# Optimization experiments

Hardware: AMD Instinct MI355X
Metric: run time of the kernel (lower is better)

## Reference

```python
import jax, jax.numpy as jnp
import numpy as np

DT = 0.01


def _mlp(x, W1, b1, W2, b2, W3, b3):
    # Linear -> tanh -> Linear -> tanh -> Linear
    h = jnp.tanh(x @ W1 + b1)
    h = jnp.tanh(h @ W2 + b2)
    return h @ W3 + b3


def setup_inputs() -> dict:
    B, T, D, H, F = 512, 128, 512, 1024, 128
    key = jax.random.key(0)
    ks = jax.random.split(key, 20)

    def lin(kw, kb, fan_in, fan_out):
        W = jax.random.normal(kw, (fan_in, fan_out), jnp.float32) / jnp.sqrt(jnp.float32(fan_in))
        b = jnp.zeros((fan_out,), jnp.float32)
        return W, b

    window = jax.random.normal(ks[0], (B, T, D), jnp.float32)
    eW1, eb1 = lin(ks[1], ks[2], D, H)
    eW2, eb2 = lin(ks[3], ks[4], H, H)
    eW3, eb3 = lin(ks[5], ks[6], H, F)
    dW1, db1 = lin(ks[7], ks[8], F, H)
    dW2, db2 = lin(ks[9], ks[10], H, H)
    dW3, db3 = lin(ks[11], ks[12], H, D)
    kW1, kb1 = lin(ks[13], ks[14], F, F)  # koopman_dim -> 2*num_eigenvalues == F
    kW2, kb2 = lin(ks[15], ks[16], F, F)
    return {
        'window': window,
        'eW1': eW1, 'eb1': eb1, 'eW2': eW2, 'eb2': eb2, 'eW3': eW3, 'eb3': eb3,
        'dW1': dW1, 'db1': db1, 'dW2': dW2, 'db2': db2, 'dW3': dW3, 'db3': db3,
        'kW1': kW1, 'kb1': kb1, 'kW2': kW2, 'kb2': kb2,
    }


def _koopman(z0, T, kW1, kb1, kW2, kb2):
    # parameterization: Linear -> tanh -> Linear, producing (mu, omega) per eigen-pair
    B, F = z0.shape
    n_eig = F // 2
    p = jnp.tanh(z0 @ kW1 + kb1) @ kW2 + kb2          # [B, 2*n_eig]
    p = p.reshape(B, n_eig, 2)
    mu, omega = p[..., 0], p[..., 1]
    exp_mu = jnp.exp(mu * DT)
    c = jnp.cos(omega * DT)
    s = jnp.sin(omega * DT)
    # per-sample 2x2 rotation-scaling blocks: [B, n_eig, 2, 2]
    blocks = jnp.stack([
        jnp.stack([exp_mu * c, -exp_mu * s], axis=-1),
        jnp.stack([exp_mu * s, exp_mu * c], axis=-1),
    ], axis=-2)

    def step(z, _):
        zp = z.reshape(B, n_eig, 2)
        zn = jnp.einsum('bnij,bnj->bni', blocks, zp).reshape(B, F)
        return zn, zn

    _, preds = jax.lax.scan(step, z0, None, length=T)  # [T, B, F]
    return jnp.transpose(preds, (1, 0, 2))             # [B, T, F]


def reference(window, eW1, eb1, eW2, eb2, eW3, eb3,
              dW1, db1, dW2, db2, dW3, db3,
              kW1, kb1, kW2, kb2):
    x0 = window[:, 0, :]          # [B, D]
    targets = window[:, 1:, :]    # [B, T-1, D]
    T = targets.shape[1]

    z0 = _mlp(x0, eW1, eb1, eW2, eb2, eW3, eb3)          # [B, F]
    x0_recon = _mlp(z0, dW1, db1, dW2, db2, dW3, db3)    # [B, D]
    z_pred = _koopman(z0, T, kW1, kb1, kW2, kb2)         # [B, T-1, F]
    x_pred = _mlp(z_pred, dW1, db1, dW2, db2, dW3, db3)  # [B, T-1, D]
    z_true = _mlp(targets, eW1, eb1, eW2, eb2, eW3, eb3) # [B, T-1, F]

    loss_recon = jnp.mean((x0_recon - x0) ** 2)
    loss_linear = jnp.mean((z_pred - z_true) ** 2)
    loss_pred = jnp.mean((x_pred - targets) ** 2)
    total = loss_recon + loss_linear + loss_pred
    return total, loss_recon, loss_linear, loss_pred
```

## Files before the change

### kernel.cpp

```cpp
#include <hip/hip_runtime.h>
#include <cstddef>
#include <cstdint>


#define KDT 0.01f
#define CH 16384
#define NCHUNK 4

typedef _Float16 f16;
typedef f16 f16x8 __attribute__((ext_vector_type(8)));
typedef f16 f16x4 __attribute__((ext_vector_type(4)));
typedef float f32x4 __attribute__((ext_vector_type(4)));

typedef __attribute__((address_space(1))) const unsigned int gu32;
typedef __attribute__((address_space(3))) unsigned int lu32;

__device__ __forceinline__ void gl_lds16(const void* g, void* l) {
    __builtin_amdgcn_global_load_lds((gu32*)g, (lu32*)l, 16, 0, 0);
}

__device__ __forceinline__ float fast_tanh(float x) {
    x = fminf(fmaxf(x, -15.f), 15.f);
    const float e = __expf(2.f * x);
    return (e - 1.f) / (e + 1.f);
}

#define PB_LIN 0
#define PB_REC 4096
#define PB_PRED 6144
#define PB_TOTAL 8192

template <int MODE, bool TANH, bool OUTF16>
__global__ __launch_bounds__(256) void k_gemm_f16(const f16* __restrict__ A,
                                                  const f16* __restrict__ Wt,
                                                  const float* __restrict__ bias,
                                                  void* __restrict__ Cv,
                                                  int M, int N, int K,
                                                  const float* __restrict__ win,
                                                  int g0,
                                                  double* __restrict__ p0,
                                                  double* __restrict__ p1)
{
    __shared__ __align__(16) f16 As[128][32];
    __shared__ __align__(16) f16 Bs[128][32];
    __shared__ double sm[256];

    const int t  = threadIdx.x;
    const int l  = t & 63;
    const int wv = t >> 6;
    const int wr = wv >> 1, wc = wv & 1;
    const int lm = l & 15, lk = l >> 4;
    const int bm = blockIdx.y, bn = blockIdx.x;

    const f16* Ab = A  + (size_t)bm * 128 * K;
    const f16* Bb = Wt + (size_t)bn * 128 * K;
    char* sA = (char*)&As[0][0];
    char* sB = (char*)&Bs[0][0];
    const int wbase = wv * 64;

    f32x4 acc[4][4] = {};

    for (int k0 = 0; k0 < K; k0 += 32) {
#pragma unroll
        for (int r = 0; r < 2; ++r) {
            const int c = r * 256 + t;
            const size_t goff = (size_t)(c >> 2) * K + (size_t)k0 + (size_t)(c & 3) * 8;
            gl_lds16(Ab + goff, sA + (size_t)(r * 256 + wbase) * 16);
            gl_lds16(Bb + goff, sB + (size_t)(r * 256 + wbase) * 16);
        }
        __syncthreads();

        f16x8 af[4], bf[4];
#pragma unroll
        for (int i = 0; i < 4; ++i) {
            af[i] = *reinterpret_cast<const f16x8*>(&As[wr * 64 + i * 16 + lm][lk * 8]);
            bf[i] = *reinterpret_cast<const f16x8*>(&Bs[wc * 64 + i * 16 + lm][lk * 8]);
        }
#pragma unroll
        for (int i = 0; i < 4; ++i)
#pragma unroll
            for (int j = 0; j < 4; ++j)
                acc[i][j] = __builtin_amdgcn_mfma_f32_16x16x32_f16(af[i], bf[j], acc[i][j], 0, 0, 0);
        __syncthreads();
    }

    const int col0 = bn * 128 + wc * 64;

    if (MODE == 0) {
        const int row0 = bm * 128 + wr * 64;
#pragma unroll
        for (int j = 0; j < 4; ++j) {
            const int col = col0 + j * 16 + lm;
            const float bv = bias[col];
#pragma unroll
            for (int i = 0; i < 4; ++i)
#pragma unroll
                for (int q = 0; q < 4; ++q) {
                    const int row = row0 + i * 16 + lk * 4 + q;
                    float v = acc[i][j][q] + bv;
                    if (TANH) v = fast_tanh(v);
                    if (OUTF16) ((f16*)Cv)[(size_t)row * N + col] = (f16)v;
                    else        ((float*)Cv)[(size_t)row * N + col] = v;
                }
        }
    } else {
        double s0 = 0.0, s1 = 0.0;
#pragma unroll
        for (int i = 0; i < 4; ++i) {
#pragma unroll
            for (int q = 0; q < 4; ++q) {
                const int rl = bm * 128 + wr * 64 + i * 16 + lk * 4 + q;
                const int g  = g0 + rl;
                const int tt = g & 127;
#pragma unroll
                for (int j = 0; j < 4; ++j) {
                    const int col = col0 + j * 16 + lm;
                    const float v = acc[i][j][q] + bias[col];
                    const float d = v - win[(size_t)g * 512 + col];
                    if (tt == 0) s0 += (double)d * d;
                    else         s1 += (double)d * d;
                }
            }
        }
        const int bid = blockIdx.y * gridDim.x + blockIdx.x;
        sm[t] = s0;
        __syncthreads();
        for (int o = 128; o > 0; o >>= 1) {
            if (t < o) sm[t] += sm[t + o];
            __syncthreads();
        }
        if (t == 0) p0[bid] = sm[0];
        __syncthreads();
        sm[t] = s1;
        __syncthreads();
        for (int o = 128; o > 0; o >>= 1) {
            if (t < o) sm[t] += sm[t + o];
            __syncthreads();
        }
        if (t == 0) p1[bid] = sm[0];
    }
}

__global__ __launch_bounds__(256) void k_wt(const float* __restrict__ W,
                                            f16* __restrict__ Wt, int K, int N)
{
    __shared__ float tl[32][33];
    const int n0 = blockIdx.x * 32, k0 = blockIdx.y * 32;
    const int tx = threadIdx.x & 31, ty = threadIdx.x >> 5;
#pragma unroll
    for (int i = 0; i < 32; i += 8)
        tl[ty + i][tx] = W[(size_t)(k0 + ty + i) * N + n0 + tx];
    __syncthreads();
#pragma unroll
    for (int i = 0; i < 32; i += 8)
        Wt[(size_t)(n0 + ty + i) * K + k0 + tx] = (f16)tl[tx][ty + i];
}

__global__ __launch_bounds__(256) void k_gather_all(const float* __restrict__ win,
                                                    f16* __restrict__ out, int g0)
{
    const int i = blockIdx.x * 256 + threadIdx.x;
    if (i >= CH * 64) return;
    const int r = i >> 6, c8 = i & 63;
    const float* s = win + ((size_t)(g0 + r)) * 512 + c8 * 8;
    const float4 v0 = *reinterpret_cast<const float4*>(s);
    const float4 v1 = *reinterpret_cast<const float4*>(s + 4);
    f16x8 o;
    o[0] = (f16)v0.x; o[1] = (f16)v0.y; o[2] = (f16)v0.z; o[3] = (f16)v0.w;
    o[4] = (f16)v1.x; o[5] = (f16)v1.y; o[6] = (f16)v1.z; o[7] = (f16)v1.w;
    *reinterpret_cast<f16x8*>(out + (size_t)r * 512 + c8 * 8) = o;
}

__global__ __launch_bounds__(256) void k_gather_z0(const float* __restrict__ cZfull,
                                                   float* __restrict__ z0f32,
                                                   f16* __restrict__ z0f16)
{
    const int i = blockIdx.x * 256 + threadIdx.x;
    if (i >= 512 * 32) return;
    const int b = i >> 5, c4 = i & 31;
    const float4 v = *reinterpret_cast<const float4*>(cZfull + (size_t)b * 16384 + c4 * 4);
    *reinterpret_cast<float4*>(z0f32 + (size_t)b * 128 + c4 * 4) = v;
    f16x4 o;
    o[0] = (f16)v.x; o[1] = (f16)v.y; o[2] = (f16)v.z; o[3] = (f16)v.w;
    *reinterpret_cast<f16x4*>(z0f16 + (size_t)b * 128 + c4 * 4) = o;
}

__global__ __launch_bounds__(256) void k_koop(const float* __restrict__ cZ,
                                              const float* __restrict__ z0,
                                              const float* __restrict__ pK,
                                              int g0,
                                              f16* __restrict__ decin,
                                              double* __restrict__ p0)
{
    const int idx = blockIdx.x * 256 + threadIdx.x;
    const int r = idx >> 4, c8 = idx & 15;
    const int g = g0 + r;
    const int tt = g & 127;
    const int bb = g >> 7;

    float zt[8];
    *reinterpret_cast<float4*>(zt)     = *reinterpret_cast<const float4*>(cZ + (size_t)r * 128 + c8 * 8);
    *reinterpret_cast<float4*>(zt + 4) = *reinterpret_cast<const float4*>(cZ + (size_t)r * 128 + c8 * 8 + 4);

    double s = 0.0;
    float ov[8];
    if (tt == 0) {
#pragma unroll
        for (int k = 0; k < 8; ++k) ov[k] = zt[k];
    } else {
        float zz[8], qq[8];
        *reinterpret_cast<float4*>(zz)     = *reinterpret_cast<const float4*>(z0 + (size_t)bb * 128 + c8 * 8);
        *reinterpret_cast<float4*>(zz + 4) = *reinterpret_cast<const float4*>(z0 + (size_t)bb * 128 + c8 * 8 + 4);
        *reinterpret_cast<float4*>(qq)     = *reinterpret_cast<const float4*>(pK + (size_t)bb * 128 + c8 * 8);
        *reinterpret_cast<float4*>(qq + 4) = *reinterpret_cast<const float4*>(pK + (size_t)bb * 128 + c8 * 8 + 4);
        const float tf = KDT * (float)tt;
#pragma unroll
        for (int pr = 0; pr < 4; ++pr) {
            const float e = __expf(qq[2 * pr] * tf);
            float sn, cs;
            __sincosf(qq[2 * pr + 1] * tf, &sn, &cs);
            const float zx = zz[2 * pr], zy = zz[2 * pr + 1];
            const float a = e * (cs * zx - sn * zy);
            const float b = e * (sn * zx + cs * zy);
            ov[2 * pr] = a; ov[2 * pr + 1] = b;
            const float d0 = a - zt[2 * pr], d1 = b - zt[2 * pr + 1];
            s += (double)d0 * d0 + (double)d1 * d1;
        }
    }
    f16x8 o;
#pragma unroll
    for (int k = 0; k < 8; ++k) o[k] = (f16)ov[k];
    *reinterpret_cast<f16x8*>(decin + (size_t)r * 128 + c8 * 8) = o;

    __shared__ double sm[256];
    sm[threadIdx.x] = s;
    __syncthreads();
    for (int off = 128; off > 0; off >>= 1) {
        if (threadIdx.x < (unsigned)off) sm[threadIdx.x] += sm[threadIdx.x + off];
        __syncthreads();
    }
    if (threadIdx.x == 0) p0[blockIdx.x] = sm[0];
}

__global__ __launch_bounds__(256) void k_finalize(const double* __restrict__ pb,
                                                  float* __restrict__ out)
{
    __shared__ double sm[256];
    const int t = threadIdx.x;
    double a0 = 0.0, a1 = 0.0, a2 = 0.0;
    for (int i = t; i < 4096; i += 256) a0 += pb[PB_LIN + i];
    for (int i = t; i < 2048; i += 256) a1 += pb[PB_REC + i];
    for (int i = t; i < 2048; i += 256) a2 += pb[PB_PRED + i];

    double r[3];
    double v[3] = {a0, a1, a2};
    for (int k = 0; k < 3; ++k) {
        sm[t] = v[k];
        __syncthreads();
        for (int o = 128; o > 0; o >>= 1) {
            if (t < o) sm[t] += sm[t + o];
            __syncthreads();
        }
        r[k] = sm[0];
        __syncthreads();
    }
    if (t == 0) {
        const double linear = r[0] / (65024.0 * 128.0);
        const double recon  = r[1] / (512.0 * 512.0);
        const double pred   = r[2] / (65024.0 * 512.0);
        out[0] = (float)(recon + linear + pred);
        out[1] = (float)recon;
        out[2] = (float)linear;
        out[3] = (float)pred;
    }
}

extern "C" void kernel_launch(void* const* d_in, const int* in_sizes, int n_in,
                              void* d_out, int out_size, void* d_ws, size_t ws_size,
                              hipStream_t stream)
{
    const float* window = (const float*)d_in[0];
    const float* eW1 = (const float*)d_in[1];
    const float* eb1 = (const float*)d_in[2];
    const float* eW2 = (const float*)d_in[3];
    const float* eb2 = (const float*)d_in[4];
    const float* eW3 = (const float*)d_in[5];
    const float* eb3 = (const float*)d_in[6];
    const float* dW1 = (const float*)d_in[7];
    const float* db1 = (const float*)d_in[8];
    const float* dW2 = (const float*)d_in[9];
    const float* db2 = (const float*)d_in[10];
    const float* dW3 = (const float*)d_in[11];
    const float* db3 = (const float*)d_in[12];
    const float* kW1 = (const float*)d_in[13];
    const float* kb1 = (const float*)d_in[14];
    const float* kW2 = (const float*)d_in[15];
    const float* kb2 = (const float*)d_in[16];
    float* out = (float*)d_out;
    (void)in_sizes; (void)n_in; (void)out_size; (void)ws_size;

    char* p = (char*)d_ws;
    size_t off = 0;
    auto takeB = [&](size_t bytes) -> char* {
        char* r = p + off;
        off += (bytes + 255) & ~(size_t)255;
        return r;
    };
    double* pb = (double*)takeB(PB_TOTAL * 8);
    f16* eW1t = (f16*)takeB((size_t)512 * 1024 * 2);
    f16* eW2t = (f16*)takeB((size_t)1024 * 1024 * 2);
    f16* eW3t = (f16*)takeB((size_t)1024 * 128 * 2);
    f16* dW1t = (f16*)takeB((size_t)128 * 1024 * 2);
    f16* dW2t = (f16*)takeB((size_t)1024 * 1024 * 2);
    f16* dW3t = (f16*)takeB((size_t)1024 * 512 * 2);
    f16* kW1t = (f16*)takeB((size_t)128 * 128 * 2);
    f16* kW2t = (f16*)takeB((size_t)128 * 128 * 2);
    float* z0f32 = (float*)takeB((size_t)65536 * 4);
    f16* z0f16 = (f16*)takeB((size_t)65536 * 2);
    f16* hK = (f16*)takeB((size_t)65536 * 2);
    float* pKbuf = (float*)takeB((size_t)65536 * 4);
    float* cZfull = (float*)takeB((size_t)65536 * 128 * 4);
    f16* cIn = (f16*)takeB((size_t)CH * 512 * 2);
    f16* cH1 = (f16*)takeB((size_t)CH * 1024 * 2);
    f16* cH2 = (f16*)takeB((size_t)CH * 1024 * 2);
    f16* decin = (f16*)takeB((size_t)CH * 128 * 2);

    hipMemsetAsync(pb, 0, PB_TOTAL * 8, stream);

    auto G = [&](const f16* A, const f16* Wt, const float* b, void* C,
                 int M, int N, int K, bool tanh_, bool f16out) {
        dim3 grid(N / 128, M / 128);
        if (tanh_)       k_gemm_f16<0, true,  true ><<<grid, 256, 0, stream>>>(A, Wt, b, C, M, N, K, nullptr, 0, nullptr, nullptr);
        else if (f16out) k_gemm_f16<0, false, true ><<<grid, 256, 0, stream>>>(A, Wt, b, C, M, N, K, nullptr, 0, nullptr, nullptr);
        else             k_gemm_f16<0, false, false><<<grid, 256, 0, stream>>>(A, Wt, b, C, M, N, K, nullptr, 0, nullptr, nullptr);
    };
    auto WT = [&](const float* W, f16* Wt, int K, int N) {
        k_wt<<<dim3(N / 32, K / 32), 256, 0, stream>>>(W, Wt, K, N);
    };

    WT(eW1, eW1t, 512, 1024);  WT(eW2, eW2t, 1024, 1024); WT(eW3, eW3t, 1024, 128);
    WT(dW1, dW1t, 128, 1024);  WT(dW2, dW2t, 1024, 1024); WT(dW3, dW3t, 1024, 512);
    WT(kW1, kW1t, 128, 128);   WT(kW2, kW2t, 128, 128);

    for (int c = 0; c < NCHUNK; ++c) {
        const int g0 = c * CH;
        k_gather_all<<<CH * 64 / 256, 256, 0, stream>>>(window, cIn, g0);
        G(cIn, eW1t, eb1, cH1, CH, 1024, 512, true, true);
        G(cH1, eW2t, eb2, cH2, CH, 1024, 1024, true, true);
        G(cH2, eW3t, eb3, cZfull + (size_t)g0 * 128, CH, 128, 1024, false, false);
    }

    k_gather_z0<<<64, 256, 0, stream>>>(cZfull, z0f32, z0f16);
    G(z0f16, kW1t, kb1, hK, 512, 128, 128, true, true);
    G(hK,    kW2t, kb2, pKbuf, 512, 128, 128, false, false);

    for (int c = 0; c < NCHUNK; ++c) {
        const int g0 = c * CH;
        k_koop<<<CH * 16 / 256, 256, 0, stream>>>(cZfull + (size_t)g0 * 128, z0f32, pKbuf,
                                                  g0, decin, pb + PB_LIN + c * 1024);
        G(decin, dW1t, db1, cH1, CH, 1024, 128, true, true);
        G(cH1,   dW2t, db2, cH2, CH, 1024, 1024, true, true);
        k_gemm_f16<2, false, false><<<dim3(4, CH / 128), 256, 0, stream>>>(
            cH2, dW3t, db3, nullptr, CH, 512, 1024,
            window, g0, pb + PB_REC + c * 512, pb + PB_PRED + c * 512);
    }

    k_finalize<<<1, 256, 0, stream>>>(pb, out);
}
```

Baseline: 1.284 ms.

## Add 256x256 double-buffered swizzled MFMA GEMM and single-chunk execution

Introduces a new 256x256-tile GEMM kernel with 512 threads, XOR-swizzled LDS layout, double-buffered global-to-LDS prefetch interleaved with MFMA phases, s_setprio around the MFMA blocks, and grid remapping for cache locality. It is used for the large encoder and decoder layers, including the fused loss epilogue. When the workspace is large enough, the whole batch runs as one chunk instead of four. The aim is more data reuse per tile, overlap of loads with compute, and fewer launches, at the cost of higher register and LDS pressure and lower occupancy.

```diff
diff --git a/kernel.cpp b/kernel.cpp
--- a/kernel.cpp
+++ b/kernel.cpp
@@ -4,8 +4,6 @@
 
 
 #define KDT 0.01f
-#define CH 16384
-#define NCHUNK 4
 
 typedef _Float16 f16;
 typedef f16 f16x8 __attribute__((ext_vector_type(8)));
@@ -30,20 +28,187 @@
 #define PB_PRED 6144
 #define PB_TOTAL 8192
 
+
+__device__ __forceinline__ void stage256(const f16* __restrict__ g, char* ldsDst,
+                                         int t, int K, int kk)
+{
+#pragma unroll
+    for (int r = 0; r < 4; ++r) {
+        const int row = r * 64 + (t >> 3);
+        const int sc = ((t & 7) ^ (row & 7)) * 8;
+        gl_lds16(g + (size_t)row * K + kk + sc, ldsDst + row * 128 + (t & 7) * 16);
+    }
+}
+
+template <int MH, int NH>
+__device__ __forceinline__ void phase_mfma(f32x4 (&acc)[8][4], const char* sA, const char* sB,
+                                           int wm, int wn, int lm, int lk)
+{
+    f16x8 af[4][2], bf[2][2];
+#pragma unroll
+    for (int i = 0; i < 4; ++i)
+#pragma unroll
+        for (int ks = 0; ks < 2; ++ks) {
+            const int row = wm * 128 + (MH * 4 + i) * 16 + lm;
+            const int slot = (ks * 4 + lk) ^ (lm & 7);
+            af[i][ks] = *(const f16x8*)(sA + row * 128 + slot * 16);
+        }
+#pragma unroll
+    for (int j = 0; j < 2; ++j)
+#pragma unroll
+        for (int ks = 0; ks < 2; ++ks) {
+            const int row = wn * 64 + (NH * 2 + j) * 16 + lm;
+            const int slot = (ks * 4 + lk) ^ (lm & 7);
+            bf[j][ks] = *(const f16x8*)(sB + row * 128 + slot * 16);
+        }
+    __builtin_amdgcn_s_setprio(1);
+#pragma unroll
+    for (int i = 0; i < 4; ++i)
+#pragma unroll
+        for (int j = 0; j < 2; ++j)
+#pragma unroll
+            for (int ks = 0; ks < 2; ++ks)
+                acc[MH * 4 + i][NH * 2 + j] = __builtin_amdgcn_mfma_f32_16x16x32_f16(
+                    af[i][ks], bf[j][ks], acc[MH * 4 + i][NH * 2 + j], 0, 0, 0);
+    __builtin_amdgcn_s_setprio(0);
+}
+
+template <bool PREF>
+__device__ __forceinline__ void run_tile(f32x4 (&acc)[8][4], char* sbase, int buf,
+                                         const f16* __restrict__ Ab, const f16* __restrict__ Bb,
+                                         int t, int K, int kkNext, int wm, int wn, int lm, int lk)
+{
+    const char* sA = sbase + buf * 32768;
+    const char* sB = sbase + 65536 + buf * 32768;
+    char* dA = sbase + (buf ^ 1) * 32768;
+    char* dB = sbase + 65536 + (buf ^ 1) * 32768;
+    phase_mfma<0, 0>(acc, sA, sB, wm, wn, lm, lk);
+    if (PREF) stage256(Ab, dA, t, K, kkNext);
+    phase_mfma<0, 1>(acc, sA, sB, wm, wn, lm, lk);
+    if (PREF) stage256(Bb, dB, t, K, kkNext);
+    phase_mfma<1, 0>(acc, sA, sB, wm, wn, lm, lk);
+    phase_mfma<1, 1>(acc, sA, sB, wm, wn, lm, lk);
+}
+
 template <int MODE, bool TANH, bool OUTF16>
+__global__ __launch_bounds__(512, 2) void k_gemm256(const f16* __restrict__ A,
+                                                    const f16* __restrict__ Wt,
+                                                    const float* __restrict__ bias,
+                                                    void* __restrict__ Cv,
+                                                    int M, int N, int K,
+                                                    const float* __restrict__ win,
+                                                    int g0,
+                                                    double* __restrict__ p0,
+                                                    double* __restrict__ p1)
+{
+    __shared__ __align__(16) f16 lds[65536];
+    char* sbase = (char*)lds;
+
+    const int t  = threadIdx.x;
+    const int l  = t & 63;
+    const int wid = t >> 6;
+    const int wm = wid >> 2, wn = wid & 3;
+    const int lm = l & 15, lk = l >> 4;
+
+    const int gx = gridDim.x;
+    const int nwg = gx * gridDim.y;
+    const int orig = blockIdx.y * gx + blockIdx.x;
+    const int cpx = nwg >> 3;
+    const int tile = (orig & 7) * cpx + (orig >> 3);
+    const int bm = tile / gx;
+    const int bn = tile % gx;
+
+    const f16* Ab = A  + (size_t)bm * 256 * K;
+    const f16* Bb = Wt + (size_t)bn * 256 * K;
+    const int nt = K >> 6;
+
+    f32x4 acc[8][4] = {};
+
+    stage256(Ab, sbase, t, K, 0);
+    stage256(Bb, sbase + 65536, t, K, 0);
+    __syncthreads();
+
+    for (int kt = 0; kt < nt; kt += 2) {
+        run_tile<true>(acc, sbase, 0, Ab, Bb, t, K, (kt + 1) << 6, wm, wn, lm, lk);
+        __syncthreads();
+        if (kt + 2 < nt) {
+            run_tile<true>(acc, sbase, 1, Ab, Bb, t, K, (kt + 2) << 6, wm, wn, lm, lk);
+            __syncthreads();
+        } else {
+            run_tile<false>(acc, sbase, 1, Ab, Bb, t, K, 0, wm, wn, lm, lk);
+        }
+    }
+
+    const int row0g = bm * 256 + wm * 128;
+    const int col0g = bn * 256 + wn * 64;
+
+    if (MODE == 0) {
+#pragma unroll
+        for (int n = 0; n < 4; ++n) {
+            const int col = col0g + n * 16 + lm;
+            const float bv = bias[col];
+#pragma unroll
+            for (int m = 0; m < 8; ++m)
+#pragma unroll
+                for (int q = 0; q < 4; ++q) {
+                    const int row = row0g + m * 16 + lk * 4 + q;
+                    float v = acc[m][n][q] + bv;
+                    if (TANH) v = fast_tanh(v);
+                    if (OUTF16) ((f16*)Cv)[(size_t)row * N + col] = (f16)v;
+                    else        ((float*)Cv)[(size_t)row * N + col] = v;
+                }
+        }
+    } else {
+        double s0 = 0.0, s1 = 0.0;
+        float bv[4];
+#pragma unroll
+        for (int n = 0; n < 4; ++n) bv[n] = bias[col0g + n * 16 + lm];
+#pragma unroll
+        for (int m = 0; m < 8; ++m)
+#pragma unroll
+            for (int q = 0; q < 4; ++q) {
+                const int rl = row0g + m * 16 + lk * 4 + q;
+                const int g  = g0 + rl;
+                const int tt = g & 127;
+#pragma unroll
+                for (int n = 0; n < 4; ++n) {
+                    const int col = col0g + n * 16 + lm;
+                    const float v = acc[m][n][q] + bv[n];
+                    const float d = v - win[(size_t)g * 512 + col];
+                    if (tt == 0) s0 += (double)d * d;
+                    else         s1 += (double)d * d;
+                }
+            }
+        __syncthreads();
+        double* dsm = (double*)lds;
+        const int slot = (g0 / 256 + bm) * gx + bn;
+        dsm[t] = s0;
+        __syncthreads();
+        for (int o = 256; o > 0; o >>= 1) {
+            if (t < o) dsm[t] += dsm[t + o];
+            __syncthreads();
+        }
+        if (t == 0) p0[slot] = dsm[0];
+        __syncthreads();
+        dsm[t] = s1;
+        __syncthreads();
+        for (int o = 256; o > 0; o >>= 1) {
+            if (t < o) dsm[t] += dsm[t + o];
+            __syncthreads();
+        }
+        if (t == 0) p1[slot] = dsm[0];
+    }
+}
+
+template <bool TANH, bool OUTF16>
 __global__ __launch_bounds__(256) void k_gemm_f16(const f16* __restrict__ A,
                                                   const f16* __restrict__ Wt,
                                                   const float* __restrict__ bias,
                                                   void* __restrict__ Cv,
-                                                  int M, int N, int K,
-                                                  const float* __restrict__ win,
-                                                  int g0,
-                                                  double* __restrict__ p0,
-                                                  double* __restrict__ p1)
+                                                  int M, int N, int K)
 {
     __shared__ __align__(16) f16 As[128][32];
     __shared__ __align__(16) f16 Bs[128][32];
-    __shared__ double sm[256];
 
     const int t  = threadIdx.x;
     const int l  = t & 63;
@@ -84,60 +249,22 @@
         __syncthreads();
     }
 
+    const int row0 = bm * 128 + wr * 64;
     const int col0 = bn * 128 + wc * 64;
-
-    if (MODE == 0) {
-        const int row0 = bm * 128 + wr * 64;
-#pragma unroll
-        for (int j = 0; j < 4; ++j) {
-            const int col = col0 + j * 16 + lm;
-            const float bv = bias[col];
-#pragma unroll
-            for (int i = 0; i < 4; ++i)
-#pragma unroll
-                for (int q = 0; q < 4; ++q) {
-                    const int row = row0 + i * 16 + lk * 4 + q;
-                    float v = acc[i][j][q] + bv;
-                    if (TANH) v = fast_tanh(v);
-                    if (OUTF16) ((f16*)Cv)[(size_t)row * N + col] = (f16)v;
-                    else        ((float*)Cv)[(size_t)row * N + col] = v;
-                }
-        }
-    } else {
-        double s0 = 0.0, s1 = 0.0;
-#pragma unroll
-        for (int i = 0; i < 4; ++i) {
+#pragma unroll
+    for (int j = 0; j < 4; ++j) {
+        const int col = col0 + j * 16 + lm;
+        const float bv = bias[col];
+#pragma unroll
+        for (int i = 0; i < 4; ++i)
 #pragma unroll
             for (int q = 0; q < 4; ++q) {
-                const int rl = bm * 128 + wr * 64 + i * 16 + lk * 4 + q;
-                const int g  = g0 + rl;
-                const int tt = g & 127;
-#pragma unroll
-                for (int j = 0; j < 4; ++j) {
-                    const int col = col0 + j * 16 + lm;
-                    const float v = acc[i][j][q] + bias[col];
-                    const float d = v - win[(size_t)g * 512 + col];
-                    if (tt == 0) s0 += (double)d * d;
-                    else         s1 += (double)d * d;
-                }
+                const int row = row0 + i * 16 + lk * 4 + q;
+                float v = acc[i][j][q] + bv;
+                if (TANH) v = fast_tanh(v);
+                if (OUTF16) ((f16*)Cv)[(size_t)row * N + col] = (f16)v;
+                else        ((float*)Cv)[(size_t)row * N + col] = v;
             }
-        }
-        const int bid = blockIdx.y * gridDim.x + blockIdx.x;
-        sm[t] = s0;
-        __syncthreads();
-        for (int o = 128; o > 0; o >>= 1) {
-            if (t < o) sm[t] += sm[t + o];
-            __syncthreads();
-        }
-        if (t == 0) p0[bid] = sm[0];
-        __syncthreads();
-        sm[t] = s1;
-        __syncthreads();
-        for (int o = 128; o > 0; o >>= 1) {
-            if (t < o) sm[t] += sm[t + o];
-            __syncthreads();
-        }
-        if (t == 0) p1[bid] = sm[0];
     }
 }
 
@@ -157,10 +284,10 @@
 }
 
 __global__ __launch_bounds__(256) void k_gather_all(const float* __restrict__ win,
-                                                    f16* __restrict__ out, int g0)
+                                                    f16* __restrict__ out, int g0, int nrows)
 {
     const int i = blockIdx.x * 256 + threadIdx.x;
-    if (i >= CH * 64) return;
+    if (i >= nrows * 64) return;
     const int r = i >> 6, c8 = i & 63;
     const float* s = win + ((size_t)(g0 + r)) * 512 + c8 * 8;
     const float4 v0 = *reinterpret_cast<const float4*>(s);
@@ -188,49 +315,51 @@
 __global__ __launch_bounds__(256) void k_koop(const float* __restrict__ cZ,
                                               const float* __restrict__ z0,
                                               const float* __restrict__ pK,
-                                              int g0,
+                                              int g0, int nrows,
                                               f16* __restrict__ decin,
                                               double* __restrict__ p0)
 {
     const int idx = blockIdx.x * 256 + threadIdx.x;
-    const int r = idx >> 4, c8 = idx & 15;
-    const int g = g0 + r;
-    const int tt = g & 127;
-    const int bb = g >> 7;
-
-    float zt[8];
-    *reinterpret_cast<float4*>(zt)     = *reinterpret_cast<const float4*>(cZ + (size_t)r * 128 + c8 * 8);
-    *reinterpret_cast<float4*>(zt + 4) = *reinterpret_cast<const float4*>(cZ + (size_t)r * 128 + c8 * 8 + 4);
-
     double s = 0.0;
-    float ov[8];
-    if (tt == 0) {
-#pragma unroll
-        for (int k = 0; k < 8; ++k) ov[k] = zt[k];
-    } else {
-        float zz[8], qq[8];
-        *reinterpret_cast<float4*>(zz)     = *reinterpret_cast<const float4*>(z0 + (size_t)bb * 128 + c8 * 8);
-        *reinterpret_cast<float4*>(zz + 4) = *reinterpret_cast<const float4*>(z0 + (size_t)bb * 128 + c8 * 8 + 4);
-        *reinterpret_cast<float4*>(qq)     = *reinterpret_cast<const float4*>(pK + (size_t)bb * 128 + c8 * 8);
-        *reinterpret_cast<float4*>(qq + 4) = *reinterpret_cast<const float4*>(pK + (size_t)bb * 128 + c8 * 8 + 4);
-        const float tf = KDT * (float)tt;
-#pragma unroll
-        for (int pr = 0; pr < 4; ++pr) {
-            const float e = __expf(qq[2 * pr] * tf);
-            float sn, cs;
-            __sincosf(qq[2 * pr + 1] * tf, &sn, &cs);
-            const float zx = zz[2 * pr], zy = zz[2 * pr + 1];
-            const float a = e * (cs * zx - sn * zy);
-            const float b = e * (sn * zx + cs * zy);
-            ov[2 * pr] = a; ov[2 * pr + 1] = b;
-            const float d0 = a - zt[2 * pr], d1 = b - zt[2 * pr + 1];
-            s += (double)d0 * d0 + (double)d1 * d1;
-        }
-    }
-    f16x8 o;
-#pragma unroll
-    for (int k = 0; k < 8; ++k) o[k] = (f16)ov[k];
-    *reinterpret_cast<f16x8*>(decin + (size_t)r * 128 + c8 * 8) = o;
+    if (idx < nrows * 16) {
+        const int r = idx >> 4, c8 = idx & 15;
+        const int g = g0 + r;
+        const int tt = g & 127;
+        const int bb = g >> 7;
+
+        float zt[8];
+        *reinterpret_cast<float4*>(zt)     = *reinterpret_cast<const float4*>(cZ + (size_t)r * 128 + c8 * 8);
+        *reinterpret_cast<float4*>(zt + 4) = *reinterpret_cast<const float4*>(cZ + (size_t)r * 128 + c8 * 8 + 4);
+
+        float ov[8];
+        if (tt == 0) {
+#pragma unroll
+            for (int k = 0; k < 8; ++k) ov[k] = zt[k];
+        } else {
+            float zz[8], qq[8];
+            *reinterpret_cast<float4*>(zz)     = *reinterpret_cast<const float4*>(z0 + (size_t)bb * 128 + c8 * 8);
+            *reinterpret_cast<float4*>(zz + 4) = *reinterpret_cast<const float4*>(z0 + (size_t)bb * 128 + c8 * 8 + 4);
+            *reinterpret_cast<float4*>(qq)     = *reinterpret_cast<const float4*>(pK + (size_t)bb * 128 + c8 * 8);
+            *reinterpret_cast<float4*>(qq + 4) = *reinterpret_cast<const float4*>(pK + (size_t)bb * 128 + c8 * 8 + 4);
+            const float tf = KDT * (float)tt;
+#pragma unroll
+            for (int pr = 0; pr < 4; ++pr) {
+                const float e = __expf(qq[2 * pr] * tf);
+                float sn, cs;
+                __sincosf(qq[2 * pr + 1] * tf, &sn, &cs);
+                const float zx = zz[2 * pr], zy = zz[2 * pr + 1];
+                const float a = e * (cs * zx - sn * zy);
+                const float b = e * (sn * zx + cs * zy);
+                ov[2 * pr] = a; ov[2 * pr + 1] = b;
+                const float d0 = a - zt[2 * pr], d1 = b - zt[2 * pr + 1];
+                s += (double)d0 * d0 + (double)d1 * d1;
+            }
+        }
+        f16x8 o;
+#pragma unroll
+        for (int k = 0; k < 8; ++k) o[k] = (f16)ov[k];
+        *reinterpret_cast<f16x8*>(decin + (size_t)r * 128 + c8 * 8) = o;
+    }
 
     __shared__ double sm[256];
     sm[threadIdx.x] = s;
@@ -297,7 +426,10 @@
     const float* kW2 = (const float*)d_in[15];
     const float* kb2 = (const float*)d_in[16];
     float* out = (float*)d_out;
-    (void)in_sizes; (void)n_in; (void)out_size; (void)ws_size;
+    (void)in_sizes; (void)n_in; (void)out_size;
+
+    const int nch = (ws_size >= (450ull << 20)) ? 1 : 4;
+    const int MC  = 65536 / nch;
 
     char* p = (char*)d_ws;
     size_t off = 0;
@@ -320,19 +452,26 @@
     f16* hK = (f16*)takeB((size_t)65536 * 2);
     float* pKbuf = (float*)takeB((size_t)65536 * 4);
     float* cZfull = (float*)takeB((size_t)65536 * 128 * 4);
-    f16* cIn = (f16*)takeB((size_t)CH * 512 * 2);
-    f16* cH1 = (f16*)takeB((size_t)CH * 1024 * 2);
-    f16* cH2 = (f16*)takeB((size_t)CH * 1024 * 2);
-    f16* decin = (f16*)takeB((size_t)CH * 128 * 2);
+    f16* aIn  = (f16*)takeB((size_t)MC * 512 * 2);
+    f16* cH1  = (f16*)takeB((size_t)MC * 1024 * 2);
+    f16* cH2  = (f16*)takeB((size_t)MC * 1024 * 2);
+    f16* decin = (f16*)takeB((size_t)MC * 128 * 2);
 
     hipMemsetAsync(pb, 0, PB_TOTAL * 8, stream);
 
-    auto G = [&](const f16* A, const f16* Wt, const float* b, void* C,
-                 int M, int N, int K, bool tanh_, bool f16out) {
+    auto G256 = [&](const f16* A, const f16* Wt, const float* b, void* C,
+                    int M, int N, int K, bool tanh_, bool f16out) {
+        dim3 grid(N / 256, M / 256);
+        if (tanh_)       k_gemm256<0, true,  true ><<<grid, 512, 0, stream>>>(A, Wt, b, C, M, N, K, nullptr, 0, nullptr, nullptr);
+        else if (f16out) k_gemm256<0, false, true ><<<grid, 512, 0, stream>>>(A, Wt, b, C, M, N, K, nullptr, 0, nullptr, nullptr);
+        else             k_gemm256<0, false, false><<<grid, 512, 0, stream>>>(A, Wt, b, C, M, N, K, nullptr, 0, nullptr, nullptr);
+    };
+    auto G128 = [&](const f16* A, const f16* Wt, const float* b, void* C,
+                    int M, int N, int K, bool tanh_, bool f16out) {
         dim3 grid(N / 128, M / 128);
-        if (tanh_)       k_gemm_f16<0, true,  true ><<<grid, 256, 0, stream>>>(A, Wt, b, C, M, N, K, nullptr, 0, nullptr, nullptr);
-        else if (f16out) k_gemm_f16<0, false, true ><<<grid, 256, 0, stream>>>(A, Wt, b, C, M, N, K, nullptr, 0, nullptr, nullptr);
-        else             k_gemm_f16<0, false, false><<<grid, 256, 0, stream>>>(A, Wt, b, C, M, N, K, nullptr, 0, nullptr, nullptr);
+        if (tanh_)       k_gemm_f16<true,  true ><<<grid, 256, 0, stream>>>(A, Wt, b, C, M, N, K);
+        else if (f16out) k_gemm_f16<false, true ><<<grid, 256, 0, stream>>>(A, Wt, b, C, M, N, K);
+        else             k_gemm_f16<false, false><<<grid, 256, 0, stream>>>(A, Wt, b, C, M, N, K);
     };
     auto WT = [&](const float* W, f16* Wt, int K, int N) {
         k_wt<<<dim3(N / 32, K / 32), 256, 0, stream>>>(W, Wt, K, N);
@@ -342,27 +481,27 @@
     WT(dW1, dW1t, 128, 1024);  WT(dW2, dW2t, 1024, 1024); WT(dW3, dW3t, 1024, 512);
     WT(kW1, kW1t, 128, 128);   WT(kW2, kW2t, 128, 128);
 
-    for (int c = 0; c < NCHUNK; ++c) {
-        const int g0 = c * CH;
-        k_gather_all<<<CH * 64 / 256, 256, 0, stream>>>(window, cIn, g0);
-        G(cIn, eW1t, eb1, cH1, CH, 1024, 512, true, true);
-        G(cH1, eW2t, eb2, cH2, CH, 1024, 1024, true, true);
-        G(cH2, eW3t, eb3, cZfull + (size_t)g0 * 128, CH, 128, 1024, false, false);
+    for (int c = 0; c < nch; ++c) {
+        const int g0 = c * MC;
+        k_gather_all<<<MC * 64 / 256, 256, 0, stream>>>(window, aIn, g0, MC);
+        G256(aIn, eW1t, eb1, cH1, MC, 1024, 512, true, true);
+        G256(cH1, eW2t, eb2, cH2, MC, 1024, 1024, true, true);
+        G128(cH2, eW3t, eb3, cZfull + (size_t)g0 * 128, MC, 128, 1024, false, false);
     }
 
     k_gather_z0<<<64, 256, 0, stream>>>(cZfull, z0f32, z0f16);
-    G(z0f16, kW1t, kb1, hK, 512, 128, 128, true, true);
-    G(hK,    kW2t, kb2, pKbuf, 512, 128, 128, false, false);
-
-    for (int c = 0; c < NCHUNK; ++c) {
-        const int g0 = c * CH;
-        k_koop<<<CH * 16 / 256, 256, 0, stream>>>(cZfull + (size_t)g0 * 128, z0f32, pKbuf,
-                                                  g0, decin, pb + PB_LIN + c * 1024);
-        G(decin, dW1t, db1, cH1, CH, 1024, 128, true, true);
-        G(cH1,   dW2t, db2, cH2, CH, 1024, 1024, true, true);
-        k_gemm_f16<2, false, false><<<dim3(4, CH / 128), 256, 0, stream>>>(
-            cH2, dW3t, db3, nullptr, CH, 512, 1024,
-            window, g0, pb + PB_REC + c * 512, pb + PB_PRED + c * 512);
+    G128(z0f16, kW1t, kb1, hK, 512, 128, 128, true, true);
+    G128(hK,    kW2t, kb2, pKbuf, 512, 128, 128, false, false);
+
+    for (int c = 0; c < nch; ++c) {
+        const int g0 = c * MC;
+        k_koop<<<MC / 16, 256, 0, stream>>>(cZfull + (size_t)g0 * 128, z0f32, pKbuf,
+                                            g0, MC, decin, pb + PB_LIN + (g0 >> 4));
+        G256(decin, dW1t, db1, cH1, MC, 1024, 128, true, true);
+        G256(cH1,   dW2t, db2, cH2, MC, 1024, 1024, true, true);
+        k_gemm256<2, false, false><<<dim3(2, MC / 256), 512, 0, stream>>>(
+            cH2, dW3t, db3, nullptr, MC, 512, 1024,
+            window, g0, pb + PB_REC, pb + PB_PRED);
     }
 
     k_finalize<<<1, 256, 0, stream>>>(pb, out);
```

New measurement: 2.963 ms. 131% more time.
